# Optimization experiments

Measured on AMD Instinct MI355X. Metric: run time of the kernel, lower is better.

## Reference

```python
import jax, jax.numpy as jnp
import numpy as np

B, L, H, I = 2, 256, 768, 1536


def setup_inputs() -> dict:
    key = jax.random.key(0)
    ks = jax.random.split(key, 10)
    s = 0.02
    return {
        "hidden_state": jax.random.normal(ks[0], (B, L, H), dtype=jnp.float32),
        "start_w": jax.random.normal(ks[1], (H,), dtype=jnp.float32) * s,
        "start_b": jnp.zeros((), dtype=jnp.float32),
        "end_w": jax.random.normal(ks[2], (H,), dtype=jnp.float32) * s,
        "end_b": jnp.zeros((), dtype=jnp.float32),
        "w1": jax.random.normal(ks[3], (2 * H, I), dtype=jnp.float32) * s,
        "b1": jnp.zeros((I,), dtype=jnp.float32),
        "w2": jax.random.normal(ks[4], (I,), dtype=jnp.float32) * s,
        "b2": jnp.zeros((), dtype=jnp.float32),
    }


def reference(hidden_state, start_w, start_b, end_w, end_b, w1, b1, w2, b2):
    # start/end token logits: (B, L)
    start_logits = jnp.einsum("blh,h->bl", hidden_state, start_w) + start_b
    end_logits = jnp.einsum("blh,h->bl", hidden_state, end_w) + end_b

    # Linear(concat(start_extend, end_extend)) == start @ w1[:H] + end @ w1[H:]
    # (algebraically identical; avoids materializing the (B,L,L,2H) concat)
    w1_start, w1_end = w1[:H], w1[H:]
    a = jnp.einsum("bsh,hi->bsi", hidden_state, w1_start)  # (B, L, I)
    c = jnp.einsum("bth,hi->bti", hidden_state, w1_end)    # (B, L, I)
    inter = jax.nn.gelu(a[:, :, None, :] + c[:, None, :, :] + b1,
                        approximate=False)                 # (B, L, L, I)
    span_logits = jnp.einsum("bsti,i->bst", inter, w2) + b2  # (B, L, L)

    return start_logits, end_logits, span_logits
```

## Files before the change

### kernel.cpp

```cpp
#include <hip/hip_runtime.h>
#include <math.h>

#define NB 2
#define NL 256
#define NH 768
#define NI 1536
#define NM (NB * NL)

typedef __attribute__((ext_vector_type(8))) short bf16x8;
typedef __attribute__((ext_vector_type(4))) float f32x4;

#if __has_builtin(__builtin_amdgcn_exp2f)
#define FAST_EXP2(x) __builtin_amdgcn_exp2f(x)
#else
#define FAST_EXP2(x) exp2f(x)
#endif
#if __has_builtin(__builtin_amdgcn_rcpf)
#define FAST_RCP(x) __builtin_amdgcn_rcpf(x)
#else
#define FAST_RCP(x) (1.0f / (x))
#endif

#define KQ (-2.4554669f)

__device__ __forceinline__ unsigned short f2bf(float f) {
  unsigned int u = __builtin_bit_cast(unsigned int, f);
  u += 0x7FFFu + ((u >> 16) & 1u);
  return (unsigned short)(u >> 16);
}
__device__ __forceinline__ unsigned int pack2(float lo, float hi) {
  return (unsigned int)f2bf(lo) | ((unsigned int)f2bf(hi) << 16);
}

__global__ __launch_bounds__(256) void logits_kernel(
    const float* __restrict__ hs,
    const float* __restrict__ sw, const float* __restrict__ sb,
    const float* __restrict__ ew, const float* __restrict__ eb,
    float* __restrict__ out) {
  int m = blockIdx.x;
  int tid = threadIdx.x;
  const float* row = hs + (size_t)m * NH;
  float accs = 0.f, acce = 0.f;
  for (int h = tid; h < NH; h += 256) {
    float v = row[h];
    accs = fmaf(v, sw[h], accs);
    acce = fmaf(v, ew[h], acce);
  }
  for (int off = 32; off > 0; off >>= 1) {
    accs += __shfl_down(accs, off, 64);
    acce += __shfl_down(acce, off, 64);
  }
  __shared__ float s_s[4], s_e[4];
  int wid = tid >> 6;
  if ((tid & 63) == 0) { s_s[wid] = accs; s_e[wid] = acce; }
  __syncthreads();
  if (tid == 0) {
    float ts = s_s[0] + s_s[1] + s_s[2] + s_s[3];
    float te = s_e[0] + s_e[1] + s_e[2] + s_e[3];
    out[m]      = ts + sb[0];
    out[NM + m] = te + eb[0];
  }
}

__global__ __launch_bounds__(512) void gemm_mfma(
    const float* __restrict__ hs, const float* __restrict__ w1,
    const float* __restrict__ b1, const float* __restrict__ w2,
    float* __restrict__ aOut, float* __restrict__ cE) {
  constexpr int BM = 64, BN = 96, BK = 32;
  __shared__ short A_lds[BM * BK];
  __shared__ short B_lds[BN * BK];

  const int mode = blockIdx.z;
  const float* __restrict__ W = w1 + (size_t)mode * NH * NI;
  const int m0 = blockIdx.x * BM;
  const int n0 = blockIdx.y * BN;
  const int tid = threadIdx.x;
  const int lane = tid & 63;
  const int wid = tid >> 6;
  const int wr = wid >> 1;
  const int wc = wid & 1;

  const int ar  = tid >> 3;
  const int ac  = (tid & 7) * 4;
  const int bkq = (tid >> 5) * 2;
  const int bnl = tid & 31;

  f32x4 acc[3] = {};

  float4 av = *reinterpret_cast<const float4*>(hs + (size_t)(m0 + ar) * NH + ac);
  float bv[2][3];
#pragma unroll
  for (int j = 0; j < 2; ++j) {
    const float* pb = W + (size_t)(bkq + j) * NI + n0 + bnl;
#pragma unroll
    for (int nn = 0; nn < 3; ++nn) bv[j][nn] = pb[nn * 32];
  }

  for (int k0 = 0; k0 < NH; k0 += BK) {
    __syncthreads();
    {
      uint2 v;
      v.x = pack2(av.x, av.y);
      v.y = pack2(av.z, av.w);
      const int off = ar * 64 + ((((ac >> 3) & 3) ^ (ar & 3)) << 4) + ((ac & 4) << 1);
      *reinterpret_cast<uint2*>(reinterpret_cast<char*>(A_lds) + off) = v;
    }
#pragma unroll
    for (int nn = 0; nn < 3; ++nn) {
      const int n = bnl + nn * 32;
      unsigned int v = pack2(bv[0][nn], bv[1][nn]);
      const int off = n * 64 + (((bkq >> 3) ^ (n & 3)) << 4) + ((bkq * 2) & 12);
      *reinterpret_cast<unsigned int*>(reinterpret_cast<char*>(B_lds) + off) = v;
    }
    __syncthreads();
    const int kn = k0 + BK;
    if (kn < NH) {
      av = *reinterpret_cast<const float4*>(hs + (size_t)(m0 + ar) * NH + kn + ac);
#pragma unroll
      for (int j = 0; j < 2; ++j) {
        const float* pb = W + (size_t)(kn + bkq + j) * NI + n0 + bnl;
#pragma unroll
        for (int nn = 0; nn < 3; ++nn) bv[j][nn] = pb[nn * 32];
      }
    }
    const int lr = lane & 15, ls = lane >> 4;
    bf16x8 af, bf[3];
    {
      const int row = wr * 16 + lr;
      const int off = row * 64 + ((ls ^ (row & 3)) << 4);
      af = *reinterpret_cast<const bf16x8*>(reinterpret_cast<const char*>(A_lds) + off);
    }
#pragma unroll
    for (int nt = 0; nt < 3; ++nt) {
      const int nrow = wc * 48 + nt * 16 + lr;
      const int off = nrow * 64 + ((ls ^ (nrow & 3)) << 4);
      bf[nt] = *reinterpret_cast<const bf16x8*>(reinterpret_cast<const char*>(B_lds) + off);
    }
#pragma unroll
    for (int nt = 0; nt < 3; ++nt)
      acc[nt] = __builtin_amdgcn_mfma_f32_16x16x32_bf16(af, bf[nt], acc[nt], 0, 0, 0);
  }

  const int lr = lane & 15, lq = lane >> 4;
  if (mode == 0) {
    const int mb = m0 + wr * 16 + lq * 4;
#pragma unroll
    for (int nt = 0; nt < 3; ++nt) {
      const int n = n0 + wc * 48 + nt * 16 + lr;
      const float bias = b1[n];
#pragma unroll
      for (int r = 0; r < 4; ++r)
        aOut[(size_t)(mb + r) * NI + n] = acc[nt][r] + bias;
    }
  } else {
    const int b = m0 >> 8;
    const int tb = (m0 & (NL - 1)) + wr * 16 + lq * 4;
#pragma unroll
    for (int nt = 0; nt < 3; ++nt) {
      const int i = n0 + wc * 48 + nt * 16 + lr;
      const float wv = w2[i];
      float* dst = cE + (((size_t)b * NI + i) * NL + tb) * 2;
      f32x4 v = acc[nt];
      float4 lo = make_float4(v[0] * wv, FAST_EXP2(KQ * v[0]),
                              v[1] * wv, FAST_EXP2(KQ * v[1]));
      float4 hi = make_float4(v[2] * wv, FAST_EXP2(KQ * v[2]),
                              v[3] * wv, FAST_EXP2(KQ * v[3]));
      *reinterpret_cast<float4*>(dst)     = lo;
      *reinterpret_cast<float4*>(dst + 4) = hi;
    }
  }
}

__global__ __launch_bounds__(256, 2) void span_kernel(
    const float* __restrict__ aRow,
    const float* __restrict__ cE,
    const float* __restrict__ w2,
    const float* __restrict__ b2,
    float* __restrict__ out) {
  const int blk = blockIdx.x;
  const int sg  = blk >> 3;
  const int te  = blk & 7;
  const int s0  = sg * 2;
  const int b   = s0 >> 8;
  const int tbase = te * 32;
  const int tid = threadIdx.x;
  const int t8  = tid & 7;
  const int q   = tid >> 3;
  const int lane = tid & 63;
  const int w    = tid >> 6;

  __shared__ float4 aw4[NI + 32];
  __shared__ float4 red[4][2][8];

  const float* a0p = aRow + (size_t)s0 * NI;
  const float* a1p = a0p + NI;
  for (int i = tid; i < NI; i += 256) {
    float a0 = a0p[i], a1 = a1p[i], wv = w2[i];
    aw4[i + i / 48] = make_float4(a0 * wv, a1 * wv,
                                  FAST_EXP2(KQ * a0), FAST_EXP2(KQ * a1));
  }
  __syncthreads();

  const float* cb = cE + (((size_t)b * NI + q * 48) * NL + tbase + t8 * 4) * 2;
  const float4* awq = aw4 + q * 49;

  f32x4 acc0 = {0.f, 0.f, 0.f, 0.f};
  f32x4 acc1 = {0.f, 0.f, 0.f, 0.f};

#pragma unroll 4
  for (int ii = 0; ii < 48; ++ii) {
    float4 cv01 = *reinterpret_cast<const float4*>(cb);
    float4 cv23 = *reinterpret_cast<const float4*>(cb + 4);
    float4 A = awq[ii];
    {
      float n0 = A.x + cv01.x, n1 = A.x + cv01.z;
      float n2 = A.x + cv23.x, n3 = A.x + cv23.z;
      float d0 = fmaf(A.z, cv01.y, 1.f), d1 = fmaf(A.z, cv01.w, 1.f);
      float d2 = fmaf(A.z, cv23.y, 1.f), d3 = fmaf(A.z, cv23.w, 1.f);
      float mA = d0 * d1, mB = d2 * d3;
      float r = FAST_RCP(mA * mB);
      float rA = r * mB, rB = r * mA;
      acc0[0] = fmaf(n0, rA * d1, acc0[0]);
      acc0[1] = fmaf(n1, rA * d0, acc0[1]);
      acc0[2] = fmaf(n2, rB * d3, acc0[2]);
      acc0[3] = fmaf(n3, rB * d2, acc0[3]);
    }
    {
      float n0 = A.y + cv01.x, n1 = A.y + cv01.z;
      float n2 = A.y + cv23.x, n3 = A.y + cv23.z;
      float d0 = fmaf(A.w, cv01.y, 1.f), d1 = fmaf(A.w, cv01.w, 1.f);
      float d2 = fmaf(A.w, cv23.y, 1.f), d3 = fmaf(A.w, cv23.w, 1.f);
      float mA = d0 * d1, mB = d2 * d3;
      float r = FAST_RCP(mA * mB);
      float rA = r * mB, rB = r * mA;
      acc1[0] = fmaf(n0, rA * d1, acc1[0]);
      acc1[1] = fmaf(n1, rA * d0, acc1[1]);
      acc1[2] = fmaf(n2, rB * d3, acc1[2]);
      acc1[3] = fmaf(n3, rB * d2, acc1[3]);
    }
    cb += NL * 2;
  }

#pragma unroll
  for (int k = 0; k < 4; ++k) {
    acc0[k] += __shfl_xor(acc0[k], 8, 64);
    acc0[k] += __shfl_xor(acc0[k], 16, 64);
    acc0[k] += __shfl_xor(acc0[k], 32, 64);
    acc1[k] += __shfl_xor(acc1[k], 8, 64);
    acc1[k] += __shfl_xor(acc1[k], 16, 64);
    acc1[k] += __shfl_xor(acc1[k], 32, 64);
  }
  if (lane < 8) {
    red[w][0][lane] = make_float4(acc0[0], acc0[1], acc0[2], acc0[3]);
    red[w][1][lane] = make_float4(acc1[0], acc1[1], acc1[2], acc1[3]);
  }
  __syncthreads();
  if (tid < 16) {
    const int s = tid >> 3;
    const int tt = tid & 7;
    float4 v0 = red[0][s][tt];
    float4 v1 = red[1][s][tt];
    float4 v2 = red[2][s][tt];
    float4 v3 = red[3][s][tt];
    const float bb = b2[0];
    float4 o;
    o.x = (v0.x + v1.x) + (v2.x + v3.x) + bb;
    o.y = (v0.y + v1.y) + (v2.y + v3.y) + bb;
    o.z = (v0.z + v1.z) + (v2.z + v3.z) + bb;
    o.w = (v0.w + v1.w) + (v2.w + v3.w) + bb;
    *reinterpret_cast<float4*>(out + 2 * NM + (size_t)(s0 + s) * NL + tbase + tt * 4) = o;
  }
}

extern "C" void kernel_launch(void* const* d_in, const int* in_sizes, int n_in,
                              void* d_out, int out_size, void* d_ws, size_t ws_size,
                              hipStream_t stream) {
  const float* hs = (const float*)d_in[0];
  const float* sw = (const float*)d_in[1];
  const float* sb = (const float*)d_in[2];
  const float* ew = (const float*)d_in[3];
  const float* eb = (const float*)d_in[4];
  const float* w1 = (const float*)d_in[5];
  const float* b1 = (const float*)d_in[6];
  const float* w2 = (const float*)d_in[7];
  const float* b2 = (const float*)d_in[8];
  float* out = (float*)d_out;

  float* a  = (float*)d_ws;
  float* cE = (float*)d_ws + (size_t)NM * NI;

  logits_kernel<<<NM, 256, 0, stream>>>(hs, sw, sb, ew, eb, out);

  dim3 ggrid(NM / 64, NI / 96, 2);
  gemm_mfma<<<ggrid, 512, 0, stream>>>(hs, w1, b1, w2, a, cE);

  span_kernel<<<2048, 256, 0, stream>>>(a, cE, w2, b2, out);
}
```

Baseline: 72.55 us.

## Pack end-side GEMM outputs as bf16 pairs and fold logits into GEMM launch

The end-side intermediate (c*w2 and exp2 term) is now stored as two bf16 halves packed into one 32-bit word instead of two fp32 values. This halves the bytes the span kernel streams per element and lets it issue one 16-byte load where it previously issued two. Separately, the start/end logits kernel is removed and its work runs as an extra z-slice of the GEMM grid, saving one launch. The cost is reduced precision in the GELU-approximation inputs, plus extra unpack bit operations inside the inner loop.

```diff
diff --git a/kernel.cpp b/kernel.cpp
--- a/kernel.cpp
+++ b/kernel.cpp
@@ -9,6 +9,7 @@
 
 typedef __attribute__((ext_vector_type(8))) short bf16x8;
 typedef __attribute__((ext_vector_type(4))) float f32x4;
+typedef __attribute__((ext_vector_type(4))) unsigned int u32x4;
 
 #if __has_builtin(__builtin_amdgcn_exp2f)
 #define FAST_EXP2(x) __builtin_amdgcn_exp2f(x)
@@ -31,50 +32,56 @@
 __device__ __forceinline__ unsigned int pack2(float lo, float hi) {
   return (unsigned int)f2bf(lo) | ((unsigned int)f2bf(hi) << 16);
 }
-
-__global__ __launch_bounds__(256) void logits_kernel(
-    const float* __restrict__ hs,
-    const float* __restrict__ sw, const float* __restrict__ sb,
-    const float* __restrict__ ew, const float* __restrict__ eb,
-    float* __restrict__ out) {
-  int m = blockIdx.x;
-  int tid = threadIdx.x;
-  const float* row = hs + (size_t)m * NH;
-  float accs = 0.f, acce = 0.f;
-  for (int h = tid; h < NH; h += 256) {
-    float v = row[h];
-    accs = fmaf(v, sw[h], accs);
-    acce = fmaf(v, ew[h], acce);
-  }
-  for (int off = 32; off > 0; off >>= 1) {
-    accs += __shfl_down(accs, off, 64);
-    acce += __shfl_down(acce, off, 64);
-  }
-  __shared__ float s_s[4], s_e[4];
-  int wid = tid >> 6;
-  if ((tid & 63) == 0) { s_s[wid] = accs; s_e[wid] = acce; }
-  __syncthreads();
-  if (tid == 0) {
-    float ts = s_s[0] + s_s[1] + s_s[2] + s_s[3];
-    float te = s_e[0] + s_e[1] + s_e[2] + s_e[3];
-    out[m]      = ts + sb[0];
-    out[NM + m] = te + eb[0];
-  }
+__device__ __forceinline__ float bits2f(unsigned int u) {
+  return __builtin_bit_cast(float, u);
 }
 
 __global__ __launch_bounds__(512) void gemm_mfma(
     const float* __restrict__ hs, const float* __restrict__ w1,
     const float* __restrict__ b1, const float* __restrict__ w2,
-    float* __restrict__ aOut, float* __restrict__ cE) {
+    const float* __restrict__ sw, const float* __restrict__ sb,
+    const float* __restrict__ ew, const float* __restrict__ eb,
+    float* __restrict__ aOut, unsigned int* __restrict__ cE,
+    float* __restrict__ out) {
   constexpr int BM = 64, BN = 96, BK = 32;
   __shared__ short A_lds[BM * BK];
   __shared__ short B_lds[BN * BK];
+  __shared__ float ls_s[4][2], ls_e[4][2];
+
+  const int tid = threadIdx.x;
+
+  if (blockIdx.z == 2) {
+    const int gid = blockIdx.x * 16 + blockIdx.y;
+    const int g = tid >> 7;
+    const int l = tid & 127;
+    const int m = gid * 4 + g;
+    const float* row = hs + (size_t)m * NH;
+    float accs = 0.f, acce = 0.f;
+    for (int h = l; h < NH; h += 128) {
+      float v = row[h];
+      accs = fmaf(v, sw[h], accs);
+      acce = fmaf(v, ew[h], acce);
+    }
+    for (int off = 32; off > 0; off >>= 1) {
+      accs += __shfl_down(accs, off, 64);
+      acce += __shfl_down(acce, off, 64);
+    }
+    if ((tid & 63) == 0) {
+      ls_s[g][(tid >> 6) & 1] = accs;
+      ls_e[g][(tid >> 6) & 1] = acce;
+    }
+    __syncthreads();
+    if (l == 0) {
+      out[m]      = ls_s[g][0] + ls_s[g][1] + sb[0];
+      out[NM + m] = ls_e[g][0] + ls_e[g][1] + eb[0];
+    }
+    return;
+  }
 
   const int mode = blockIdx.z;
   const float* __restrict__ W = w1 + (size_t)mode * NH * NI;
   const int m0 = blockIdx.x * BM;
   const int n0 = blockIdx.y * BN;
-  const int tid = threadIdx.x;
   const int lane = tid & 63;
   const int wid = tid >> 6;
   const int wr = wid >> 1;
@@ -159,21 +166,21 @@
     for (int nt = 0; nt < 3; ++nt) {
       const int i = n0 + wc * 48 + nt * 16 + lr;
       const float wv = w2[i];
-      float* dst = cE + (((size_t)b * NI + i) * NL + tb) * 2;
+      unsigned int* dst = cE + ((size_t)b * NI + i) * NL + tb;
       f32x4 v = acc[nt];
-      float4 lo = make_float4(v[0] * wv, FAST_EXP2(KQ * v[0]),
-                              v[1] * wv, FAST_EXP2(KQ * v[1]));
-      float4 hi = make_float4(v[2] * wv, FAST_EXP2(KQ * v[2]),
-                              v[3] * wv, FAST_EXP2(KQ * v[3]));
-      *reinterpret_cast<float4*>(dst)     = lo;
-      *reinterpret_cast<float4*>(dst + 4) = hi;
+      u32x4 pk;
+      pk.x = pack2(v[0] * wv, FAST_EXP2(KQ * v[0]));
+      pk.y = pack2(v[1] * wv, FAST_EXP2(KQ * v[1]));
+      pk.z = pack2(v[2] * wv, FAST_EXP2(KQ * v[2]));
+      pk.w = pack2(v[3] * wv, FAST_EXP2(KQ * v[3]));
+      *reinterpret_cast<u32x4*>(dst) = pk;
     }
   }
 }
 
 __global__ __launch_bounds__(256, 2) void span_kernel(
     const float* __restrict__ aRow,
-    const float* __restrict__ cE,
+    const unsigned int* __restrict__ cE,
     const float* __restrict__ w2,
     const float* __restrict__ b2,
     float* __restrict__ out) {
@@ -201,7 +208,7 @@
   }
   __syncthreads();
 
-  const float* cb = cE + (((size_t)b * NI + q * 48) * NL + tbase + t8 * 4) * 2;
+  const unsigned int* cb = cE + ((size_t)b * NI + q * 48) * NL + tbase + t8 * 4;
   const float4* awq = aw4 + q * 49;
 
   f32x4 acc0 = {0.f, 0.f, 0.f, 0.f};
@@ -209,14 +216,17 @@
 
 #pragma unroll 4
   for (int ii = 0; ii < 48; ++ii) {
-    float4 cv01 = *reinterpret_cast<const float4*>(cb);
-    float4 cv23 = *reinterpret_cast<const float4*>(cb + 4);
+    u32x4 cv = *reinterpret_cast<const u32x4*>(cb);
     float4 A = awq[ii];
+    float cw0 = bits2f(cv.x << 16), E0 = bits2f(cv.x & 0xFFFF0000u);
+    float cw1 = bits2f(cv.y << 16), E1 = bits2f(cv.y & 0xFFFF0000u);
+    float cw2 = bits2f(cv.z << 16), E2 = bits2f(cv.z & 0xFFFF0000u);
+    float cw3 = bits2f(cv.w << 16), E3 = bits2f(cv.w & 0xFFFF0000u);
     {
-      float n0 = A.x + cv01.x, n1 = A.x + cv01.z;
-      float n2 = A.x + cv23.x, n3 = A.x + cv23.z;
-      float d0 = fmaf(A.z, cv01.y, 1.f), d1 = fmaf(A.z, cv01.w, 1.f);
-      float d2 = fmaf(A.z, cv23.y, 1.f), d3 = fmaf(A.z, cv23.w, 1.f);
+      float n0 = A.x + cw0, n1 = A.x + cw1;
+      float n2 = A.x + cw2, n3 = A.x + cw3;
+      float d0 = fmaf(A.z, E0, 1.f), d1 = fmaf(A.z, E1, 1.f);
+      float d2 = fmaf(A.z, E2, 1.f), d3 = fmaf(A.z, E3, 1.f);
       float mA = d0 * d1, mB = d2 * d3;
       float r = FAST_RCP(mA * mB);
       float rA = r * mB, rB = r * mA;
@@ -226,10 +236,10 @@
       acc0[3] = fmaf(n3, rB * d2, acc0[3]);
     }
     {
-      float n0 = A.y + cv01.x, n1 = A.y + cv01.z;
-      float n2 = A.y + cv23.x, n3 = A.y + cv23.z;
-      float d0 = fmaf(A.w, cv01.y, 1.f), d1 = fmaf(A.w, cv01.w, 1.f);
-      float d2 = fmaf(A.w, cv23.y, 1.f), d3 = fmaf(A.w, cv23.w, 1.f);
+      float n0 = A.y + cw0, n1 = A.y + cw1;
+      float n2 = A.y + cw2, n3 = A.y + cw3;
+      float d0 = fmaf(A.w, E0, 1.f), d1 = fmaf(A.w, E1, 1.f);
+      float d2 = fmaf(A.w, E2, 1.f), d3 = fmaf(A.w, E3, 1.f);
       float mA = d0 * d1, mB = d2 * d3;
       float r = FAST_RCP(mA * mB);
       float rA = r * mB, rB = r * mA;
@@ -238,7 +248,7 @@
       acc1[2] = fmaf(n2, rB * d3, acc1[2]);
       acc1[3] = fmaf(n3, rB * d2, acc1[3]);
     }
-    cb += NL * 2;
+    cb += NL;
   }
 
 #pragma unroll
@@ -286,13 +296,11 @@
   const float* b2 = (const float*)d_in[8];
   float* out = (float*)d_out;
 
-  float* a  = (float*)d_ws;
-  float* cE = (float*)d_ws + (size_t)NM * NI;
-
-  logits_kernel<<<NM, 256, 0, stream>>>(hs, sw, sb, ew, eb, out);
-
-  dim3 ggrid(NM / 64, NI / 96, 2);
-  gemm_mfma<<<ggrid, 512, 0, stream>>>(hs, w1, b1, w2, a, cE);
+  float* a = (float*)d_ws;
+  unsigned int* cE = (unsigned int*)((float*)d_ws + (size_t)NM * NI);
+
+  dim3 ggrid(NM / 64, NI / 96, 3);
+  gemm_mfma<<<ggrid, 512, 0, stream>>>(hs, w1, b1, w2, sw, sb, ew, eb, a, cE, out);
 
   span_kernel<<<2048, 256, 0, stream>>>(a, cE, w2, b2, out);
 }
```

Measured after the change: 62.05 us (median of 2 runs). 1.17x faster.
